# Kernel tuning notes

Hardware: AMD Instinct MI355X
Metric: run time of the kernel (lower is better)

## Reference

```python
import jax, jax.numpy as jnp
import numpy as np

N_NODES = 50000
D_IN = 256      # input_rep
D_HID = 256     # num_neurons
N_EDGES = 1600000
N_SAMPLES = 100000


def setup_inputs() -> dict:
    key = jax.random.key(0)
    ks = jax.random.split(key, 12)
    x_feature = jax.random.normal(ks[0], (N_NODES, D_IN), dtype=jnp.float32)
    edge_index = jax.random.randint(ks[1], (2, N_EDGES), 0, N_NODES, dtype=jnp.int64)
    samples = jax.random.randint(ks[2], (N_SAMPLES, 2), 0, N_NODES, dtype=jnp.int64)
    s1 = 1.0 / np.sqrt(D_IN)
    s2 = 1.0 / np.sqrt(D_HID)
    W1 = jax.random.uniform(ks[3], (D_IN, D_HID), jnp.float32, -s1, s1)
    b1 = jax.random.uniform(ks[4], (D_HID,), jnp.float32, -s1, s1)
    W2 = jax.random.uniform(ks[5], (D_HID, D_HID), jnp.float32, -s2, s2)
    b2 = jax.random.uniform(ks[6], (D_HID,), jnp.float32, -s2, s2)
    lin1_W = jax.random.uniform(ks[7], (D_IN, D_IN), jnp.float32, -s1, s1)
    lin1_b = jax.random.uniform(ks[8], (D_IN,), jnp.float32, -s1, s1)
    lin2_W = jax.random.uniform(ks[9], (D_IN, 2), jnp.float32, -s1, s1)
    lin2_b = jax.random.uniform(ks[10], (2,), jnp.float32, -s1, s1)
    return {"x_feature": x_feature, "edge_index": edge_index, "samples": samples,
            "W1": W1, "b1": b1, "W2": W2, "b2": b2,
            "lin1_W": lin1_W, "lin1_b": lin1_b, "lin2_W": lin2_W, "lin2_b": lin2_b}


def _gnn_layer(x, src, dst, W, b, n_nodes):
    # sum-aggregate neighbor messages, then linear (standard GCN-style layer)
    agg = jax.ops.segment_sum(x[src], dst, num_segments=n_nodes)  # [N, d]
    return agg @ W + b


def reference(x_feature, edge_index, samples, W1, b1, W2, b2, lin1_W, lin1_b, lin2_W, lin2_b):
    src, dst = edge_index[0], edge_index[1]
    n = x_feature.shape[0]
    # GNN stack (note: its output is discarded in the original forward; kept for faithfulness)
    h = jax.nn.relu(_gnn_layer(x_feature, src, dst, W1, b1, n))
    h = jax.nn.relu(_gnn_layer(h, src, dst, W2, b2, n))
    # fused gather + elementwise multiply over sampled pairs (replaces per-edge Python loop)
    z = x_feature[samples[:, 0]] * x_feature[samples[:, 1]]  # [S, D_IN]
    z = jax.nn.relu(z @ lin1_W + lin1_b)
    return z @ lin2_W + lin2_b  # [S, 2]
```

## Files before the change

### kernel.cpp

```cpp
#include <hip/hip_runtime.h>

typedef __attribute__((ext_vector_type(8))) short bf16x8;
typedef __attribute__((ext_vector_type(4))) float f32x4;

__device__ __forceinline__ unsigned int f2bf(float f) {
    union { float f; unsigned int u; } v; v.f = f;
    unsigned int u = v.u;
    u += 0x7FFFu + ((u >> 16) & 1u);
    return u >> 16;
}

__global__ void pack_w_kernel(const float* __restrict__ W, unsigned short* __restrict__ P) {
    int tid = blockIdx.x * blockDim.x + threadIdx.x;
    if (tid >= 8192) return;
    int f    = tid >> 9;
    int kt   = (tid >> 6) & 7;
    int lane = tid & 63;
    int k0  = kt * 32 + (lane >> 4) * 8;
    int col = f * 16 + (lane & 15);
    bf16x8 v;
    #pragma unroll
    for (int j = 0; j < 8; ++j)
        v[j] = (short)f2bf(W[(k0 + j) * 256 + col]);
    ((bf16x8*)P)[tid] = v;
}

__global__ __launch_bounds__(256, 4)
void fused_kernel(const float* __restrict__ x,
                  const int* __restrict__ samples,
                  const unsigned short* __restrict__ Wp,
                  const float* __restrict__ b1,
                  const float* __restrict__ w2,
                  const float* __restrict__ b2,
                  float* __restrict__ out, int S)
{
    __shared__ unsigned short zt[4][16][264];

    const int tid  = threadIdx.x;
    const int lane = tid & 63;
    const int wave = tid >> 6;
    const int row0 = blockIdx.x * 64 + wave * 16;
    const int cl   = lane & 15;
    const int hi   = lane >> 4;

    int sidx;
    {
        int i    = row0 * 2 + (lane & 31);
        int imax = 2 * S - 1;
        sidx = samples[i < imax ? i : imax];
    }

    #pragma unroll
    for (int g = 0; g < 4; ++g) {
        f32x4 va[4], vb[4];
        #pragma unroll
        for (int r = 0; r < 4; ++r) {
            int a = __shfl(sidx, (g * 4 + r) * 2,     64);
            int b = __shfl(sidx, (g * 4 + r) * 2 + 1, 64);
            va[r] = ((const f32x4*)x)[(size_t)a * 64 + lane];
            vb[r] = ((const f32x4*)x)[(size_t)b * 64 + lane];
        }
        #pragma unroll
        for (int r = 0; r < 4; ++r) {
            uint2 u;
            u.x = f2bf(va[r][0] * vb[r][0]) | (f2bf(va[r][1] * vb[r][1]) << 16);
            u.y = f2bf(va[r][2] * vb[r][2]) | (f2bf(va[r][3] * vb[r][3]) << 16);
            *(uint2*)&zt[wave][g * 4 + r][lane * 4] = u;
        }
    }

    bf16x8 af[8];
    #pragma unroll
    for (int kt = 0; kt < 8; ++kt)
        af[kt] = *(const bf16x8*)&zt[wave][cl][kt * 32 + hi * 8];

    const bf16x8* wg = (const bf16x8*)Wp + lane;
    float p0[4] = {0.f, 0.f, 0.f, 0.f};
    float p1[4] = {0.f, 0.f, 0.f, 0.f};

    bf16x8 bc[8];
    #pragma unroll
    for (int kt = 0; kt < 8; ++kt) bc[kt] = wg[kt * 64];

    #pragma unroll
    for (int f = 0; f < 16; ++f) {
        bf16x8 bn[8];
        if (f < 15) {
            #pragma unroll
            for (int kt = 0; kt < 8; ++kt) bn[kt] = wg[(f + 1) * 512 + kt * 64];
        }
        f32x4 a4 = (f32x4){0.f, 0.f, 0.f, 0.f};
        #pragma unroll
        for (int kt = 0; kt < 8; ++kt)
            a4 = __builtin_amdgcn_mfma_f32_16x16x32_bf16(af[kt], bc[kt], a4, 0, 0, 0);

        float  b1v = b1[f * 16 + cl];
        float2 lw  = ((const float2*)w2)[f * 16 + cl];
        #pragma unroll
        for (int q = 0; q < 4; ++q) {
            float h = fmaxf(a4[q] + b1v, 0.f);
            p0[q] += h * lw.x;
            p1[q] += h * lw.y;
        }
        #pragma unroll
        for (int kt = 0; kt < 8; ++kt) bc[kt] = bn[kt];
    }

    #pragma unroll
    for (int m = 1; m < 16; m <<= 1) {
        #pragma unroll
        for (int q = 0; q < 4; ++q) {
            p0[q] += __shfl_xor(p0[q], m, 64);
            p1[q] += __shfl_xor(p1[q], m, 64);
        }
    }
    if (cl < 8) {
        int q = cl >> 1, j = cl & 1;
        int r = row0 + hi * 4 + q;
        if (r < S) {
            float v = (j == 0 ? p0[q] : p1[q]) + b2[j];
            out[r * 2 + j] = v;
        }
    }
}

extern "C" void kernel_launch(void* const* d_in, const int* in_sizes, int n_in,
                              void* d_out, int out_size, void* d_ws, size_t ws_size,
                              hipStream_t stream) {
    const float* x       = (const float*)d_in[0];
    const int*   samples = (const int*)d_in[2];
    const float* lin1_W  = (const float*)d_in[7];
    const float* lin1_b  = (const float*)d_in[8];
    const float* lin2_W  = (const float*)d_in[9];
    const float* lin2_b  = (const float*)d_in[10];
    float* out = (float*)d_out;

    unsigned short* Wp = (unsigned short*)d_ws;
    const int S = in_sizes[2] / 2;

    pack_w_kernel<<<32, 256, 0, stream>>>(lin1_W, Wp);

    const int nblk = (S + 63) / 64;
    fused_kernel<<<nblk, 256, 0, stream>>>(x, samples, Wp, lin1_b, lin2_W, lin2_b, out, S);
}
```

Measured before the change: 62.62 us.

## Stage packed weights in LDS double buffer and build A fragments directly in registers

Weights were previously streamed by every wave from global memory. Now the block loads them cooperatively into a double-buffered shared-memory staging area, two 16-column slices per chunk, with a __syncthreads after each chunk. The gathered products are also computed straight into MFMA A-fragment registers in fragment layout, which removes the LDS transpose. This cuts redundant global and L2 weight traffic per block. In exchange it adds eight block-wide barriers, 32KB of LDS, and gather loads that are less coalesced (each lane reads 32-byte pieces of rows).

```diff
diff --git a/kernel.cpp b/kernel.cpp
--- a/kernel.cpp
+++ b/kernel.cpp
@@ -34,76 +34,87 @@
                   const float* __restrict__ b2,
                   float* __restrict__ out, int S)
 {
-    __shared__ unsigned short zt[4][16][264];
+    __shared__ bf16x8 wbuf[2][1024];
 
     const int tid  = threadIdx.x;
     const int lane = tid & 63;
     const int wave = tid >> 6;
-    const int row0 = blockIdx.x * 64 + wave * 16;
     const int cl   = lane & 15;
     const int hi   = lane >> 4;
+    const int row0 = blockIdx.x * 64 + wave * 16;
 
-    int sidx;
+    const bf16x8* wpv = (const bf16x8*)Wp;
+
+    bf16x8 st[4];
+    #pragma unroll
+    for (int i = 0; i < 4; ++i) st[i] = wpv[i * 256 + tid];
+
+    int imax = 2 * S - 1;
+    int i0   = row0 * 2 + (lane & 31);
+    int sidx = samples[i0 < imax ? i0 : imax];
+    int ra = __shfl(sidx, 2 * cl,     64);
+    int rb = __shfl(sidx, 2 * cl + 1, 64);
+    const f32x4* xa = (const f32x4*)x + (size_t)ra * 64;
+    const f32x4* xb = (const f32x4*)x + (size_t)rb * 64;
+
+    bf16x8 af[8];
     {
-        int i    = row0 * 2 + (lane & 31);
-        int imax = 2 * S - 1;
-        sidx = samples[i < imax ? i : imax];
+        f32x4 va[8][2], vb[8][2];
+        #pragma unroll
+        for (int kt = 0; kt < 8; ++kt) {
+            int o = kt * 8 + hi * 2;
+            va[kt][0] = xa[o];  va[kt][1] = xa[o + 1];
+            vb[kt][0] = xb[o];  vb[kt][1] = xb[o + 1];
+        }
+        #pragma unroll
+        for (int kt = 0; kt < 8; ++kt) {
+            bf16x8 v;
+            #pragma unroll
+            for (int j = 0; j < 4; ++j) {
+                v[j]     = (short)f2bf(va[kt][0][j] * vb[kt][0][j]);
+                v[4 + j] = (short)f2bf(va[kt][1][j] * vb[kt][1][j]);
+            }
+            af[kt] = v;
+        }
     }
 
     #pragma unroll
-    for (int g = 0; g < 4; ++g) {
-        f32x4 va[4], vb[4];
-        #pragma unroll
-        for (int r = 0; r < 4; ++r) {
-            int a = __shfl(sidx, (g * 4 + r) * 2,     64);
-            int b = __shfl(sidx, (g * 4 + r) * 2 + 1, 64);
-            va[r] = ((const f32x4*)x)[(size_t)a * 64 + lane];
-            vb[r] = ((const f32x4*)x)[(size_t)b * 64 + lane];
-        }
-        #pragma unroll
-        for (int r = 0; r < 4; ++r) {
-            uint2 u;
-            u.x = f2bf(va[r][0] * vb[r][0]) | (f2bf(va[r][1] * vb[r][1]) << 16);
-            u.y = f2bf(va[r][2] * vb[r][2]) | (f2bf(va[r][3] * vb[r][3]) << 16);
-            *(uint2*)&zt[wave][g * 4 + r][lane * 4] = u;
-        }
-    }
+    for (int i = 0; i < 4; ++i) wbuf[0][i * 256 + tid] = st[i];
+    __syncthreads();
 
-    bf16x8 af[8];
-    #pragma unroll
-    for (int kt = 0; kt < 8; ++kt)
-        af[kt] = *(const bf16x8*)&zt[wave][cl][kt * 32 + hi * 8];
-
-    const bf16x8* wg = (const bf16x8*)Wp + lane;
     float p0[4] = {0.f, 0.f, 0.f, 0.f};
     float p1[4] = {0.f, 0.f, 0.f, 0.f};
 
-    bf16x8 bc[8];
-    #pragma unroll
-    for (int kt = 0; kt < 8; ++kt) bc[kt] = wg[kt * 64];
-
-    #pragma unroll
-    for (int f = 0; f < 16; ++f) {
-        bf16x8 bn[8];
-        if (f < 15) {
+    for (int c = 0; c < 8; ++c) {
+        if (c < 7) {
             #pragma unroll
-            for (int kt = 0; kt < 8; ++kt) bn[kt] = wg[(f + 1) * 512 + kt * 64];
+            for (int i = 0; i < 4; ++i) st[i] = wpv[(c + 1) * 1024 + i * 256 + tid];
         }
-        f32x4 a4 = (f32x4){0.f, 0.f, 0.f, 0.f};
+        const bf16x8* cb = wbuf[c & 1];
         #pragma unroll
-        for (int kt = 0; kt < 8; ++kt)
-            a4 = __builtin_amdgcn_mfma_f32_16x16x32_bf16(af[kt], bc[kt], a4, 0, 0, 0);
-
-        float  b1v = b1[f * 16 + cl];
-        float2 lw  = ((const float2*)w2)[f * 16 + cl];
-        #pragma unroll
-        for (int q = 0; q < 4; ++q) {
-            float h = fmaxf(a4[q] + b1v, 0.f);
-            p0[q] += h * lw.x;
-            p1[q] += h * lw.y;
+        for (int s = 0; s < 2; ++s) {
+            int f = 2 * c + s;
+            bf16x8 bc[8];
+            #pragma unroll
+            for (int kt = 0; kt < 8; ++kt) bc[kt] = cb[s * 512 + kt * 64 + lane];
+            f32x4 a4 = (f32x4){0.f, 0.f, 0.f, 0.f};
+            #pragma unroll
+            for (int kt = 0; kt < 8; ++kt)
+                a4 = __builtin_amdgcn_mfma_f32_16x16x32_bf16(af[kt], bc[kt], a4, 0, 0, 0);
+            float  b1v = b1[f * 16 + cl];
+            float2 lw  = ((const float2*)w2)[f * 16 + cl];
+            #pragma unroll
+            for (int q = 0; q < 4; ++q) {
+                float h = fmaxf(a4[q] + b1v, 0.f);
+                p0[q] += h * lw.x;
+                p1[q] += h * lw.y;
+            }
         }
-        #pragma unroll
-        for (int kt = 0; kt < 8; ++kt) bc[kt] = bn[kt];
+        if (c < 7) {
+            #pragma unroll
+            for (int i = 0; i < 4; ++i) wbuf[(c + 1) & 1][i * 256 + tid] = st[i];
+        }
+        __syncthreads();
     }
 
     #pragma unroll
```

Result: slower. 85.38 us (+36.3%).

## Process two 16-row tiles per wave and build MFMA A-fragments directly in registers

Applied to the files above, without the earlier changes.

Each wave now handles 32 sample rows instead of 16, so every loaded B fragment of the packed weight feeds two MFMAs, halving weight traffic per row. Gathered x rows are loaded straight into the MFMA A-operand layout and converted to bf16 in registers, which removes the LDS staging buffer and its write/read round trip. The weight prefetch is restructured to reuse the bc registers after the MFMAs, and launch bounds drop to 3 waves/SIMD to allow more registers. The trade-off is more register pressure and lower occupancy, which leaves fewer waves in flight to hide the latency of the random row gathers.

```diff
diff --git a/kernel.cpp b/kernel.cpp
--- a/kernel.cpp
+++ b/kernel.cpp
@@ -25,7 +25,7 @@
     ((bf16x8*)P)[tid] = v;
 }
 
-__global__ __launch_bounds__(256, 4)
+__global__ __launch_bounds__(256, 3)
 void fused_kernel(const float* __restrict__ x,
                   const int* __restrict__ samples,
                   const unsigned short* __restrict__ Wp,
@@ -34,93 +34,103 @@
                   const float* __restrict__ b2,
                   float* __restrict__ out, int S)
 {
-    __shared__ unsigned short zt[4][16][264];
-
     const int tid  = threadIdx.x;
     const int lane = tid & 63;
     const int wave = tid >> 6;
-    const int row0 = blockIdx.x * 64 + wave * 16;
     const int cl   = lane & 15;
     const int hi   = lane >> 4;
+    const int row0 = blockIdx.x * 128 + wave * 32;
 
-    int sidx;
-    {
-        int i    = row0 * 2 + (lane & 31);
-        int imax = 2 * S - 1;
-        sidx = samples[i < imax ? i : imax];
-    }
+    const bf16x8* wgl = (const bf16x8*)Wp + lane;
 
+    bf16x8 bc[8];
+    #pragma unroll
+    for (int kt = 0; kt < 8; ++kt) bc[kt] = wgl[kt * 64];
+
+    int imax = 2 * S - 1;
+    int i0   = row0 * 2 + lane;
+    int sidx = samples[i0 < imax ? i0 : imax];
+    int ra0 = __shfl(sidx, 2 * cl,      64);
+    int rb0 = __shfl(sidx, 2 * cl + 1,  64);
+    int ra1 = __shfl(sidx, 2 * cl + 32, 64);
+    int rb1 = __shfl(sidx, 2 * cl + 33, 64);
+    const f32x4* xa0 = (const f32x4*)x + (size_t)ra0 * 64;
+    const f32x4* xb0 = (const f32x4*)x + (size_t)rb0 * 64;
+    const f32x4* xa1 = (const f32x4*)x + (size_t)ra1 * 64;
+    const f32x4* xb1 = (const f32x4*)x + (size_t)rb1 * 64;
+
+    bf16x8 af0[8], af1[8];
     #pragma unroll
     for (int g = 0; g < 4; ++g) {
-        f32x4 va[4], vb[4];
+        f32x4 v[16];
         #pragma unroll
-        for (int r = 0; r < 4; ++r) {
-            int a = __shfl(sidx, (g * 4 + r) * 2,     64);
-            int b = __shfl(sidx, (g * 4 + r) * 2 + 1, 64);
-            va[r] = ((const f32x4*)x)[(size_t)a * 64 + lane];
-            vb[r] = ((const f32x4*)x)[(size_t)b * 64 + lane];
+        for (int k = 0; k < 2; ++k) {
+            int kt = g * 2 + k;
+            int o  = kt * 8 + hi * 2;
+            v[k * 8 + 0] = xa0[o];  v[k * 8 + 1] = xa0[o + 1];
+            v[k * 8 + 2] = xb0[o];  v[k * 8 + 3] = xb0[o + 1];
+            v[k * 8 + 4] = xa1[o];  v[k * 8 + 5] = xa1[o + 1];
+            v[k * 8 + 6] = xb1[o];  v[k * 8 + 7] = xb1[o + 1];
         }
         #pragma unroll
-        for (int r = 0; r < 4; ++r) {
-            uint2 u;
-            u.x = f2bf(va[r][0] * vb[r][0]) | (f2bf(va[r][1] * vb[r][1]) << 16);
-            u.y = f2bf(va[r][2] * vb[r][2]) | (f2bf(va[r][3] * vb[r][3]) << 16);
-            *(uint2*)&zt[wave][g * 4 + r][lane * 4] = u;
+        for (int k = 0; k < 2; ++k) {
+            int kt = g * 2 + k;
+            bf16x8 u0, u1;
+            #pragma unroll
+            for (int j = 0; j < 4; ++j) {
+                u0[j]     = (short)f2bf(v[k*8+0][j] * v[k*8+2][j]);
+                u0[4 + j] = (short)f2bf(v[k*8+1][j] * v[k*8+3][j]);
+                u1[j]     = (short)f2bf(v[k*8+4][j] * v[k*8+6][j]);
+                u1[4 + j] = (short)f2bf(v[k*8+5][j] * v[k*8+7][j]);
+            }
+            af0[kt] = u0;
+            af1[kt] = u1;
         }
     }
 
-    bf16x8 af[8];
-    #pragma unroll
-    for (int kt = 0; kt < 8; ++kt)
-        af[kt] = *(const bf16x8*)&zt[wave][cl][kt * 32 + hi * 8];
-
-    const bf16x8* wg = (const bf16x8*)Wp + lane;
-    float p0[4] = {0.f, 0.f, 0.f, 0.f};
-    float p1[4] = {0.f, 0.f, 0.f, 0.f};
-
-    bf16x8 bc[8];
-    #pragma unroll
-    for (int kt = 0; kt < 8; ++kt) bc[kt] = wg[kt * 64];
+    float p00[4] = {0.f,0.f,0.f,0.f}, p10[4] = {0.f,0.f,0.f,0.f};
+    float p01[4] = {0.f,0.f,0.f,0.f}, p11[4] = {0.f,0.f,0.f,0.f};
 
     #pragma unroll
     for (int f = 0; f < 16; ++f) {
-        bf16x8 bn[8];
+        f32x4 a0 = (f32x4){0.f,0.f,0.f,0.f};
+        f32x4 a1 = (f32x4){0.f,0.f,0.f,0.f};
+        #pragma unroll
+        for (int kt = 0; kt < 8; ++kt) {
+            a0 = __builtin_amdgcn_mfma_f32_16x16x32_bf16(af0[kt], bc[kt], a0, 0, 0, 0);
+            a1 = __builtin_amdgcn_mfma_f32_16x16x32_bf16(af1[kt], bc[kt], a1, 0, 0, 0);
+        }
         if (f < 15) {
             #pragma unroll
-            for (int kt = 0; kt < 8; ++kt) bn[kt] = wg[(f + 1) * 512 + kt * 64];
+            for (int kt = 0; kt < 8; ++kt) bc[kt] = wgl[(f + 1) * 512 + kt * 64];
         }
-        f32x4 a4 = (f32x4){0.f, 0.f, 0.f, 0.f};
-        #pragma unroll
-        for (int kt = 0; kt < 8; ++kt)
-            a4 = __builtin_amdgcn_mfma_f32_16x16x32_bf16(af[kt], bc[kt], a4, 0, 0, 0);
-
         float  b1v = b1[f * 16 + cl];
         float2 lw  = ((const float2*)w2)[f * 16 + cl];
         #pragma unroll
         for (int q = 0; q < 4; ++q) {
-            float h = fmaxf(a4[q] + b1v, 0.f);
-            p0[q] += h * lw.x;
-            p1[q] += h * lw.y;
+            float h0 = fmaxf(a0[q] + b1v, 0.f);
+            float h1 = fmaxf(a1[q] + b1v, 0.f);
+            p00[q] += h0 * lw.x;  p10[q] += h0 * lw.y;
+            p01[q] += h1 * lw.x;  p11[q] += h1 * lw.y;
         }
-        #pragma unroll
-        for (int kt = 0; kt < 8; ++kt) bc[kt] = bn[kt];
     }
 
     #pragma unroll
     for (int m = 1; m < 16; m <<= 1) {
         #pragma unroll
         for (int q = 0; q < 4; ++q) {
-            p0[q] += __shfl_xor(p0[q], m, 64);
-            p1[q] += __shfl_xor(p1[q], m, 64);
+            p00[q] += __shfl_xor(p00[q], m, 64);
+            p10[q] += __shfl_xor(p10[q], m, 64);
+            p01[q] += __shfl_xor(p01[q], m, 64);
+            p11[q] += __shfl_xor(p11[q], m, 64);
         }
     }
     if (cl < 8) {
         int q = cl >> 1, j = cl & 1;
-        int r = row0 + hi * 4 + q;
-        if (r < S) {
-            float v = (j == 0 ? p0[q] : p1[q]) + b2[j];
-            out[r * 2 + j] = v;
-        }
+        int r0 = row0 + hi * 4 + q;
+        if (r0 < S) out[r0 * 2 + j] = (j == 0 ? p00[q] : p10[q]) + b2[j];
+        int r1 = row0 + 16 + hi * 4 + q;
+        if (r1 < S) out[r1 * 2 + j] = (j == 0 ? p01[q] : p11[q]) + b2[j];
     }
 }
 
@@ -140,6 +150,6 @@
 
     pack_w_kernel<<<32, 256, 0, stream>>>(lin1_W, Wp);
 
-    const int nblk = (S + 63) / 64;
+    const int nblk = (S + 127) / 128;
     fused_kernel<<<nblk, 256, 0, stream>>>(x, samples, Wp, lin1_b, lin2_W, lin2_b, out, S);
 }
```

Result: slower. 110.8 us (+76.9%).
